# Optimization experiments

Measured on AMD Instinct MI355X. Metric: run time of the kernel, lower is better.

Reference implementation:

```python
import jax, jax.numpy as jnp
import numpy as np

D = 6          # atom_dims
K_AA = 17      # atom-atom knn (self dropped -> 16)
K_PE = 16      # point-atom knn
NEG = 0.2      # LeakyReLU slope
EPS = 1e-5     # GroupNorm eps
N_PTS, N_AT = 20000, 8000
H = 2 * D + 1  # MLP hidden width = 13


def lrelu(x):
    return jnp.where(x >= 0, x, NEG * x)


def linear(x, w, b):  # torch Linear convention: w is (out, in)
    return jnp.einsum('...i,oi->...o', x, w) + b


def group_norm(x, gamma, beta, groups):
    n, c = x.shape
    xg = x.reshape(n, groups, c // groups)
    mu = xg.mean(-1, keepdims=True)
    var = ((xg - mu) ** 2).mean(-1, keepdims=True)
    xn = ((xg - mu) * jax.lax.rsqrt(var + EPS)).reshape(n, c)
    return xn * gamma + beta


def knn(x, y, k):
    # squared euclidean distances via gram trick (memory-bound argKmin)
    d2 = jnp.sum(x * x, -1)[:, None] + jnp.sum(y * y, -1)[None, :] - 2.0 * (x @ y.T)
    _, idx = jax.lax.top_k(-jax.lax.stop_gradient(d2), k)
    # recompute dists from gathered coords (matches knn_atoms; differentiable)
    dists = jnp.sum((x[:, None, :] - y[idx]) ** 2, -1)  # (N, k)
    return idx, dists


def mp_block(self_feat, nb_source, idx, dists, w1, b1, w2, b2, gamma, beta, groups):
    n, k = idx.shape
    nb = nb_source[idx]  # (N, k, D) gather
    feat = jnp.concatenate([
        jnp.broadcast_to(self_feat[:, None, :], (n, k, self_feat.shape[1])),
        nb,
        dists[..., None],
    ], axis=-1)  # (N, k, 2D+1)
    msg = linear(lrelu(linear(feat, w1, b1)), w2, b2).sum(1)  # (N, D)
    return self_feat + lrelu(group_norm(msg, gamma, beta, groups))


def setup_inputs() -> dict:
    key = jax.random.key(0)
    ks = jax.random.split(key, 20)
    f = lambda k, s, sc=1.0: jax.random.normal(k, s, jnp.float32) * sc
    inp = {
        'xyz': f(ks[0], (N_PTS, 3), 10.0),
        'atom_xyz': f(ks[1], (N_AT, 3), 10.0),
        'atomtypes': f(ks[2], (N_AT, D)),
        'batch': jnp.zeros((N_PTS,), jnp.int32),
        'atom_batch': jnp.zeros((N_AT,), jnp.int32),
        # transform_types: Linear(D,D) -> LeakyReLU -> Linear(D,D)
        'tt_w1': f(ks[3], (D, D), 0.3), 'tt_b1': f(ks[4], (D,), 0.1),
        'tt_w2': f(ks[5], (D, D), 0.3), 'tt_b2': f(ks[6], (D,), 0.1),
        # atom_atom: 3 layers of Linear(13,13)->LeakyReLU->Linear(13,6), GroupNorm(2,6)
        'aa_w1': f(ks[7], (3, H, H), 0.3), 'aa_b1': f(ks[8], (3, H), 0.1),
        'aa_w2': f(ks[9], (3, D, H), 0.3), 'aa_b2': f(ks[10], (3, D), 0.1),
        'aa_gamma': jnp.ones((3, D), jnp.float32), 'aa_beta': jnp.zeros((3, D), jnp.float32),
        # embed: same shapes
        'em_w1': f(ks[11], (3, H, H), 0.3), 'em_b1': f(ks[12], (3, H), 0.1),
        'em_w2': f(ks[13], (3, D, H), 0.3), 'em_b2': f(ks[14], (3, D), 0.1),
        'em_gamma': jnp.ones((3, D), jnp.float32), 'em_beta': jnp.zeros((3, D), jnp.float32),
    }
    return inp


def reference(xyz, atom_xyz, atomtypes, batch, atom_batch,
              tt_w1, tt_b1, tt_w2, tt_b2,
              aa_w1, aa_b1, aa_w2, aa_b2, aa_gamma, aa_beta,
              em_w1, em_b1, em_w2, em_b2, em_gamma, em_beta):
    # batch / atom_batch are all-zero (single block), so full knn == ranged knn
    at = linear(lrelu(linear(atomtypes, tt_w1, tt_b1)), tt_w2, tt_b2)
    # Atom_Atom_embedding_MP: knn over atoms, drop self (first) neighbor
    idx, dists = knn(atom_xyz, atom_xyz, K_AA)
    idx, dists = idx[:, 1:], dists[:, 1:]
    out = at
    for i in range(3):
        out = mp_block(out, out, idx, dists,
                       aa_w1[i], aa_b1[i], aa_w2[i], aa_b2[i],
                       aa_gamma[i], aa_beta[i], 2)
    # Atom_embedding_MP: points gather from (fixed) atom features
    idx2, dists2 = knn(xyz, atom_xyz, K_PE)
    emb = jnp.ones((xyz.shape[0], D), xyz.dtype)
    for i in range(3):
        emb = mp_block(emb, out, idx2, dists2,
                       em_w1[i], em_b1[i], em_w2[i], em_b2[i],
                       em_gamma[i], em_beta[i], 2)
    return emb
```

## Files before the change

kernel.cpp:

```cpp
#include <hip/hip_runtime.h>
#include <cfloat>
#include <climits>

#define NEG 0.2f
#define GEPS 1e-5f
#define D 6
#define H 13
#define KOUT 16

#define MPAD 8192
#define TILE 1024
#define NTILES 8
#define QW 8
#define QBLK 32
#define CAP 64
#define KMAX 17
#define MARGIN 0.05f

__device__ __forceinline__ float lrelu(float x){ return x >= 0.f ? x : NEG*x; }

__global__ void pack_kernel(const float* __restrict__ xyz,
                            float4* __restrict__ P, int n, int npad){
  int i = blockIdx.x*blockDim.x + threadIdx.x;
  if (i >= npad) return;
  if (i < n){
    float x = xyz[3*i], y = xyz[3*i+1], z = xyz[3*i+2];
    float sq;
    {
#pragma clang fp contract(off)
      sq = (x*x + y*y) + z*z;
    }
    P[i] = make_float4(x,y,z,sq);
  } else {
    P[i] = make_float4(0.f,0.f,0.f,1e30f);
  }
}

__global__ void tt_kernel(const float* __restrict__ at_in,
                          const float* __restrict__ w1, const float* __restrict__ b1,
                          const float* __restrict__ w2, const float* __restrict__ b2,
                          float* __restrict__ out, int n){
  int i = blockIdx.x*blockDim.x + threadIdx.x;
  if (i >= n) return;
  float x[D], h[D];
  #pragma unroll
  for (int j=0;j<D;j++) x[j] = at_in[i*D+j];
  #pragma unroll
  for (int o=0;o<D;o++){
    float acc = b1[o];
    #pragma unroll
    for (int j=0;j<D;j++) acc += w1[o*D+j]*x[j];
    h[o] = lrelu(acc);
  }
  #pragma unroll
  for (int o=0;o<D;o++){
    float acc = b2[o];
    #pragma unroll
    for (int j=0;j<D;j++) acc += w2[o*D+j]*h[j];
    out[i*D+o] = acc;
  }
}

__device__ __forceinline__ void sort64fq(float (&v)[QW], int lane){
  #pragma unroll
  for (int k = 2; k <= 64; k <<= 1){
    #pragma unroll
    for (int j = k >> 1; j >= 1; j >>= 1){
      bool dir = ((lane & j) == 0) == ((lane & k) == 0);
      #pragma unroll
      for (int q = 0; q < QW; ++q){
        float o = __shfl_xor(v[q], j);
        v[q] = dir ? fminf(v[q], o) : fmaxf(v[q], o);
      }
    }
  }
}

__device__ __forceinline__ void sort64pair(float& d, int& i, int lane){
  #pragma unroll
  for (int k = 2; k <= 64; k <<= 1){
    #pragma unroll
    for (int j = k >> 1; j >= 1; j >>= 1){
      float od = __shfl_xor(d, j);
      int   oi = __shfl_xor(i, j);
      bool lower = (lane & j) == 0;
      bool asc   = (lane & k) == 0;
      bool oless = (od < d) || (od == d && oi < i);
      bool take  = (lower == asc) ? oless : !oless;
      d = take ? od : d;
      i = take ? oi : i;
    }
  }
}

__global__ __launch_bounds__(256)
void knn9_kernel(const float4* __restrict__ candP, int ncand,
                 const float4* __restrict__ qarrA, int nqA, int nbA,
                 const float4* __restrict__ qarrB, int nqB,
                 int* __restrict__ oidxA, float* __restrict__ odistA,
                 int* __restrict__ oidxB, float* __restrict__ odistB){
  __shared__ float4 tile[TILE];
  __shared__ float4 qs[QBLK];
  __shared__ ushort slots[4][QW][CAP];
  __shared__ int    scnt[4][QW];

  const int tid  = threadIdx.x;
  const int w    = tid >> 6;
  const int lane = tid & 63;

  const bool taskA = (int)blockIdx.x < nbA;
  const int  bq    = taskA ? blockIdx.x : (blockIdx.x - nbA);
  const float4* __restrict__ qarr = taskA ? qarrA : qarrB;
  const int  nq    = taskA ? nqA : nqB;
  const int  ksel  = taskA ? 17 : 16;
  const int  ooff  = taskA ? 1  : 0;
  int*   __restrict__ oidx  = taskA ? oidxA  : oidxB;
  float* __restrict__ odist = taskA ? odistA : odistB;

  if (tid < QBLK){
    int qg = bq*QBLK + tid;
    qs[tid] = qarr[qg < nq ? qg : nq-1];
  }
  if (lane < QW) scnt[w][lane] = 0;
  __syncthreads();

  float q2x[QW], q2y[QW], q2z[QW];
  #pragma unroll
  for (int q = 0; q < QW; ++q){
    float4 v = qs[w*QW + q];
    q2x[q] = -2.f*v.x; q2y[q] = -2.f*v.y; q2z[q] = -2.f*v.z;
  }

  float mn[QW];
  #pragma unroll
  for (int q = 0; q < QW; ++q) mn[q] = FLT_MAX;

  for (int t = 0; t < NTILES; ++t){
    #pragma unroll
    for (int u = 0; u < TILE/256; ++u)
      tile[tid + 256*u] = candP[t*TILE + tid + 256*u];
    __syncthreads();
    #pragma unroll 2
    for (int i = 0; i < TILE/64; ++i){
      float4 cv = tile[i*64 + lane];
      #pragma unroll
      for (int q = 0; q < QW; ++q){
        float e = fmaf(q2x[q], cv.x, fmaf(q2y[q], cv.y, fmaf(q2z[q], cv.z, cv.w)));
        mn[q] = fminf(mn[q], e);
      }
    }
    __syncthreads();
  }

  sort64fq(mn, lane);
  float T[QW];
  #pragma unroll
  for (int q = 0; q < QW; ++q) T[q] = __shfl(mn[q], ksel-1) + MARGIN;

  for (int t = 0; t < NTILES; ++t){
    #pragma unroll
    for (int u = 0; u < TILE/256; ++u)
      tile[tid + 256*u] = candP[t*TILE + tid + 256*u];
    __syncthreads();
    #pragma unroll 2
    for (int i = 0; i < TILE/64; ++i){
      float4 cv = tile[i*64 + lane];
      const int j = t*TILE + i*64 + lane;
      #pragma unroll
      for (int q = 0; q < QW; ++q){
        float e = fmaf(q2x[q], cv.x, fmaf(q2y[q], cv.y, fmaf(q2z[q], cv.z, cv.w)));
        if (e <= T[q]){
          int ofs = atomicAdd(&scnt[w][q], 1);
          if (ofs < CAP) slots[w][q][ofs] = (ushort)j;
        }
      }
    }
    __syncthreads();
  }

  for (int q = 0; q < QW; ++q){
    const int qgq = bq*QBLK + w*QW + q;
    if (qgq >= nq) continue;
    const float4 qv = qs[w*QW + q];
    const int C = scnt[w][q];

    if (C <= CAP){
      int g = INT_MAX; float d2 = FLT_MAX;
      if (lane < C){
        g = slots[w][q][lane];
        float4 cp = candP[g];
        {
#pragma clang fp contract(off)
          float dot = qv.x*cp.x + qv.y*cp.y + qv.z*cp.z;
          d2 = (qv.w + cp.w) - 2.0f*dot;
        }
      }
      sort64pair(d2, g, lane);
      if (lane >= ooff && lane < ooff + KOUT){
        float4 cp = candP[g];
        float dist;
        {
#pragma clang fp contract(off)
          float dx = qv.x-cp.x, dy = qv.y-cp.y, dz = qv.z-cp.z;
          dist = (dx*dx + dy*dy) + dz*dz;
        }
        oidx[(size_t)qgq*KOUT + (lane-ooff)]  = g;
        odist[(size_t)qgq*KOUT + (lane-ooff)] = dist;
      }
    } else if (lane == 0){
      float bd[KMAX]; int bi[KMAX];
      for (int t=0;t<ksel;t++){ bd[t]=FLT_MAX; bi[t]=INT_MAX; }
      float cmd = FLT_MAX; int cmi = INT_MAX;
      for (int jj = 0; jj < ncand; ++jj){
        float4 cp = candP[jj];
        float d2;
        {
#pragma clang fp contract(off)
          float dot = qv.x*cp.x + qv.y*cp.y + qv.z*cp.z;
          d2 = (qv.w + cp.w) - 2.0f*dot;
        }
        if (d2 < cmd || (d2 == cmd && jj < cmi)){
          int rt = 0; float rmd=-FLT_MAX; int rmi=-1;
          for (int t=0;t<ksel;t++){
            if (bd[t] > rmd || (bd[t]==rmd && bi[t]>rmi)){ rmd=bd[t]; rmi=bi[t]; rt=t; }
          }
          bd[rt]=d2; bi[rt]=jj;
          cmd=-FLT_MAX; cmi=-1;
          for (int t=0;t<ksel;t++){
            if (bd[t] > cmd || (bd[t]==cmd && bi[t]>cmi)){ cmd=bd[t]; cmi=bi[t]; }
          }
        }
      }
      for (int t=0;t<ksel;t++){
        int rt=-1; float mnd=FLT_MAX; int mni=INT_MAX;
        for (int u2=0;u2<ksel;u2++){
          if (bd[u2] < mnd || (bd[u2]==mnd && bi[u2]<mni)){ mnd=bd[u2]; mni=bi[u2]; rt=u2; }
        }
        bd[rt]=FLT_MAX; bi[rt]=INT_MAX;
        if (t >= ooff){
          float4 cp = candP[mni];
          float dist;
          {
#pragma clang fp contract(off)
            float dx=qv.x-cp.x, dy=qv.y-cp.y, dz=qv.z-cp.z;
            dist = (dx*dx + dy*dy) + dz*dz;
          }
          oidx[(size_t)qgq*KOUT + (t-ooff)]  = mni;
          odist[(size_t)qgq*KOUT + (t-ooff)] = dist;
        }
      }
    }
  }
}

template<bool SELF_ONES>
__global__ __launch_bounds__(256)
void mp_kernel(const float* __restrict__ self_feat,
               const float* __restrict__ nb_src,
               const int* __restrict__ idx,
               const float* __restrict__ dists,
               const float* __restrict__ w1g, const float* __restrict__ b1g,
               const float* __restrict__ w2g, const float* __restrict__ b2g,
               const float* __restrict__ gam, const float* __restrict__ bet,
               float* __restrict__ out, int n){
  __shared__ float w1[H*H], b1v[H], w2[D*H], b2v[D], gm[D], bt[D];
  for (int t=threadIdx.x; t<H*H; t+=blockDim.x) w1[t]=w1g[t];
  if (threadIdx.x < H) b1v[threadIdx.x]=b1g[threadIdx.x];
  for (int t=threadIdx.x; t<D*H; t+=blockDim.x) w2[t]=w2g[t];
  if (threadIdx.x < D){
    b2v[threadIdx.x]=b2g[threadIdx.x];
    gm[threadIdx.x]=gam[threadIdx.x];
    bt[threadIdx.x]=bet[threadIdx.x];
  }
  __syncthreads();
  int tt = blockIdx.x*blockDim.x + threadIdx.x;
  int p = tt >> 2, sub = tt & 3;
  if (p >= n) return;

  float s[D];
  #pragma unroll
  for (int j=0;j<D;j++) s[j] = SELF_ONES ? 1.0f : self_feat[p*D+j];
  float msg[D] = {0,0,0,0,0,0};

  #pragma unroll
  for (int u=0;u<KOUT/4;u++){
    int k = u*4 + sub;
    int j = idx[p*KOUT+k];
    float dd = dists[p*KOUT+k];
    float f[H];
    #pragma unroll
    for (int c=0;c<D;c++) f[c]=s[c];
    #pragma unroll
    for (int c=0;c<D;c++) f[D+c]=nb_src[j*D+c];
    f[2*D]=dd;
    float h[H];
    #pragma unroll
    for (int o=0;o<H;o++){
      float acc=b1v[o];
      #pragma unroll
      for (int c=0;c<H;c++) acc += w1[o*H+c]*f[c];
      h[o]=lrelu(acc);
    }
    #pragma unroll
    for (int o=0;o<D;o++){
      float acc=b2v[o];
      #pragma unroll
      for (int c=0;c<H;c++) acc += w2[o*H+c]*h[c];
      msg[o]+=acc;
    }
  }

  #pragma unroll
  for (int c=0;c<D;c++){
    msg[c] += __shfl_xor(msg[c], 1);
    msg[c] += __shfl_xor(msg[c], 2);
  }

  if (sub == 0){
    float y[D];
    #pragma unroll
    for (int gi=0; gi<2; gi++){
      float m0=msg[gi*3+0], m1=msg[gi*3+1], m2=msg[gi*3+2];
      float mu = ((m0+m1)+m2) / 3.0f;
      float d0=m0-mu, d1=m1-mu, d2v=m2-mu;
      float var = ((d0*d0 + d1*d1) + d2v*d2v) / 3.0f;
      float inv = 1.0f / sqrtf(var + GEPS);
      y[gi*3+0] = d0*inv;
      y[gi*3+1] = d1*inv;
      y[gi*3+2] = d2v*inv;
    }
    #pragma unroll
    for (int c=0;c<D;c++){
      float vv = y[c]*gm[c] + bt[c];
      out[p*D+c] = s[c] + lrelu(vv);
    }
  }
}

extern "C" void kernel_launch(void* const* d_in, const int* in_sizes, int n_in,
                              void* d_out, int out_size, void* d_ws, size_t ws_size,
                              hipStream_t stream){
  const float* xyz       = (const float*)d_in[0];
  const float* atom_xyz  = (const float*)d_in[1];
  const float* atomtypes = (const float*)d_in[2];
  const float* tt_w1 = (const float*)d_in[5];
  const float* tt_b1 = (const float*)d_in[6];
  const float* tt_w2 = (const float*)d_in[7];
  const float* tt_b2 = (const float*)d_in[8];
  const float* aa_w1 = (const float*)d_in[9];
  const float* aa_b1 = (const float*)d_in[10];
  const float* aa_w2 = (const float*)d_in[11];
  const float* aa_b2 = (const float*)d_in[12];
  const float* aa_gamma = (const float*)d_in[13];
  const float* aa_beta  = (const float*)d_in[14];
  const float* em_w1 = (const float*)d_in[15];
  const float* em_b1 = (const float*)d_in[16];
  const float* em_w2 = (const float*)d_in[17];
  const float* em_b2 = (const float*)d_in[18];
  const float* em_gamma = (const float*)d_in[19];
  const float* em_beta  = (const float*)d_in[20];

  const int n_pts = in_sizes[0]/3;
  const int n_at  = in_sizes[1]/3;

  char* ws = (char*)d_ws;
  float4* candP = (float4*)ws; ws += (size_t)MPAD*sizeof(float4);
  float4* ptsP  = (float4*)ws; ws += (size_t)n_pts*sizeof(float4);
  float* fa   = (float*)ws; ws += (size_t)n_at*D*4;
  float* fb   = (float*)ws; ws += (size_t)n_at*D*4;
  int*   idxA = (int*)ws;   ws += (size_t)n_at*KOUT*4;
  float* distA= (float*)ws; ws += (size_t)n_at*KOUT*4;
  int*   idxP = (int*)ws;   ws += (size_t)n_pts*KOUT*4;
  float* distP= (float*)ws; ws += (size_t)n_pts*KOUT*4;
  float* ea   = (float*)ws; ws += (size_t)n_pts*D*4;
  float* eb   = (float*)ws; ws += (size_t)n_pts*D*4;
  float* outf = (float*)d_out;

  pack_kernel<<<(MPAD+255)/256,256,0,stream>>>(atom_xyz, candP, n_at, MPAD);
  pack_kernel<<<(n_pts+255)/256,256,0,stream>>>(xyz, ptsP, n_pts, n_pts);

  tt_kernel<<<(n_at+255)/256,256,0,stream>>>(atomtypes, tt_w1,tt_b1,tt_w2,tt_b2, fa, n_at);

  const int nbA = (n_at  + QBLK - 1) / QBLK;
  const int nbB = (n_pts + QBLK - 1) / QBLK;
  knn9_kernel<<<nbA + nbB,256,0,stream>>>(
      candP, n_at, candP, n_at, nbA, ptsP, n_pts,
      idxA, distA, idxP, distP);

  mp_kernel<false><<<(n_at*4+255)/256,256,0,stream>>>(fa, fa, idxA, distA,
      aa_w1+0*H*H, aa_b1+0*H, aa_w2+0*D*H, aa_b2+0*D, aa_gamma+0*D, aa_beta+0*D, fb, n_at);
  mp_kernel<false><<<(n_at*4+255)/256,256,0,stream>>>(fb, fb, idxA, distA,
      aa_w1+1*H*H, aa_b1+1*H, aa_w2+1*D*H, aa_b2+1*D, aa_gamma+1*D, aa_beta+1*D, fa, n_at);
  mp_kernel<false><<<(n_at*4+255)/256,256,0,stream>>>(fa, fa, idxA, distA,
      aa_w1+2*H*H, aa_b1+2*H, aa_w2+2*D*H, aa_b2+2*D, aa_gamma+2*D, aa_beta+2*D, fb, n_at);

  mp_kernel<true ><<<(n_pts*4+255)/256,256,0,stream>>>(nullptr, fb, idxP, distP,
      em_w1+0*H*H, em_b1+0*H, em_w2+0*D*H, em_b2+0*D, em_gamma+0*D, em_beta+0*D, ea, n_pts);
  mp_kernel<false><<<(n_pts*4+255)/256,256,0,stream>>>(ea, fb, idxP, distP,
      em_w1+1*H*H, em_b1+1*H, em_w2+1*D*H, em_b2+1*D, em_gamma+1*D, em_beta+1*D, eb, n_pts);
  mp_kernel<false><<<(n_pts*4+255)/256,256,0,stream>>>(eb, fb, idxP, distP,
      em_w1+2*H*H, em_b1+2*H, em_w2+2*D*H, em_b2+2*D, em_gamma+2*D, em_beta+2*D, outf, n_pts);
}
```

Baseline: 162.9 us.

## Bound kNN threshold from half the candidates, add exact overflow fallback, fuse prep kernels

The first kNN pass now computes its per-query min-threshold from only the first 4 of 8 candidate tiles. That still gives a valid upper bound on the k-th distance but admits more candidates. When a query's candidate count overflows the slot capacity, a new per-query fallback rescans all candidates, computes an exact threshold, and compacts the survivors with ballot. The pack and type-transform kernels are merged into one prep kernel to save launches. The trade-off is cheaper pass 1 against a looser threshold, which makes overflow and the slow fallback path more likely.

```diff
diff --git a/kernel.cpp b/kernel.cpp
--- a/kernel.cpp
+++ b/kernel.cpp
@@ -11,6 +11,7 @@
 #define MPAD 8192
 #define TILE 1024
 #define NTILES 8
+#define P1TILES 4
 #define QW 8
 #define QBLK 32
 #define CAP 64
@@ -19,45 +20,54 @@
 
 __device__ __forceinline__ float lrelu(float x){ return x >= 0.f ? x : NEG*x; }
 
-__global__ void pack_kernel(const float* __restrict__ xyz,
-                            float4* __restrict__ P, int n, int npad){
+__global__ void prep_kernel(const float* __restrict__ atom_xyz,
+                            const float* __restrict__ xyz,
+                            const float* __restrict__ at_in,
+                            const float* __restrict__ w1, const float* __restrict__ b1,
+                            const float* __restrict__ w2, const float* __restrict__ b2,
+                            float4* __restrict__ candP, float4* __restrict__ ptsP,
+                            float* __restrict__ fa, int n_at, int n_pts){
   int i = blockIdx.x*blockDim.x + threadIdx.x;
-  if (i >= npad) return;
-  if (i < n){
+  if (i < MPAD){
+    if (i < n_at){
+      float x = atom_xyz[3*i], y = atom_xyz[3*i+1], z = atom_xyz[3*i+2];
+      float sq;
+      {
+#pragma clang fp contract(off)
+        sq = (x*x + y*y) + z*z;
+      }
+      candP[i] = make_float4(x,y,z,sq);
+    } else {
+      candP[i] = make_float4(0.f,0.f,0.f,1e30f);
+    }
+  }
+  if (i < n_pts){
     float x = xyz[3*i], y = xyz[3*i+1], z = xyz[3*i+2];
     float sq;
     {
 #pragma clang fp contract(off)
       sq = (x*x + y*y) + z*z;
     }
-    P[i] = make_float4(x,y,z,sq);
-  } else {
-    P[i] = make_float4(0.f,0.f,0.f,1e30f);
-  }
-}
-
-__global__ void tt_kernel(const float* __restrict__ at_in,
-                          const float* __restrict__ w1, const float* __restrict__ b1,
-                          const float* __restrict__ w2, const float* __restrict__ b2,
-                          float* __restrict__ out, int n){
-  int i = blockIdx.x*blockDim.x + threadIdx.x;
-  if (i >= n) return;
-  float x[D], h[D];
-  #pragma unroll
-  for (int j=0;j<D;j++) x[j] = at_in[i*D+j];
-  #pragma unroll
-  for (int o=0;o<D;o++){
-    float acc = b1[o];
-    #pragma unroll
-    for (int j=0;j<D;j++) acc += w1[o*D+j]*x[j];
-    h[o] = lrelu(acc);
-  }
-  #pragma unroll
-  for (int o=0;o<D;o++){
-    float acc = b2[o];
-    #pragma unroll
-    for (int j=0;j<D;j++) acc += w2[o*D+j]*h[j];
-    out[i*D+o] = acc;
+    ptsP[i] = make_float4(x,y,z,sq);
+  }
+  if (i < n_at){
+    float x[D], h[D];
+    #pragma unroll
+    for (int j=0;j<D;j++) x[j] = at_in[i*D+j];
+    #pragma unroll
+    for (int o=0;o<D;o++){
+      float acc = b1[o];
+      #pragma unroll
+      for (int j=0;j<D;j++) acc += w1[o*D+j]*x[j];
+      h[o] = lrelu(acc);
+    }
+    #pragma unroll
+    for (int o=0;o<D;o++){
+      float acc = b2[o];
+      #pragma unroll
+      for (int j=0;j<D;j++) acc += w2[o*D+j]*h[j];
+      fa[i*D+o] = acc;
+    }
   }
 }
 
@@ -72,6 +82,18 @@
         float o = __shfl_xor(v[q], j);
         v[q] = dir ? fminf(v[q], o) : fmaxf(v[q], o);
       }
+    }
+  }
+}
+
+__device__ __forceinline__ void sort64f1(float& a, int lane){
+  #pragma unroll
+  for (int k=2;k<=64;k<<=1){
+    #pragma unroll
+    for (int j=k>>1;j>=1;j>>=1){
+      float o = __shfl_xor(a, j);
+      bool dir = ((lane&j)==0)==((lane&k)==0);
+      a = dir ? fminf(a,o) : fmaxf(a,o);
     }
   }
 }
@@ -94,11 +116,11 @@
 }
 
 __global__ __launch_bounds__(256)
-void knn9_kernel(const float4* __restrict__ candP, int ncand,
-                 const float4* __restrict__ qarrA, int nqA, int nbA,
-                 const float4* __restrict__ qarrB, int nqB,
-                 int* __restrict__ oidxA, float* __restrict__ odistA,
-                 int* __restrict__ oidxB, float* __restrict__ odistB){
+void knn10_kernel(const float4* __restrict__ candP, int ncand,
+                  const float4* __restrict__ qarrA, int nqA, int nbA,
+                  const float4* __restrict__ qarrB, int nqB,
+                  int* __restrict__ oidxA, float* __restrict__ odistA,
+                  int* __restrict__ oidxB, float* __restrict__ odistB){
   __shared__ float4 tile[TILE];
   __shared__ float4 qs[QBLK];
   __shared__ ushort slots[4][QW][CAP];
@@ -135,7 +157,7 @@
   #pragma unroll
   for (int q = 0; q < QW; ++q) mn[q] = FLT_MAX;
 
-  for (int t = 0; t < NTILES; ++t){
+  for (int t = 0; t < P1TILES; ++t){
     #pragma unroll
     for (int u = 0; u < TILE/256; ++u)
       tile[tid + 256*u] = candP[t*TILE + tid + 256*u];
@@ -182,7 +204,34 @@
     const int qgq = bq*QBLK + w*QW + q;
     if (qgq >= nq) continue;
     const float4 qv = qs[w*QW + q];
-    const int C = scnt[w][q];
+    int C = scnt[w][q];
+
+    if (C > CAP){
+      const float fq2x = -2.f*qv.x, fq2y = -2.f*qv.y, fq2z = -2.f*qv.z;
+      float m = FLT_MAX;
+      for (int j = lane; j < MPAD; j += 64){
+        float4 cp = candP[j];
+        float e = fmaf(fq2x, cp.x, fmaf(fq2y, cp.y, fmaf(fq2z, cp.z, cp.w)));
+        m = fminf(m, e);
+      }
+      sort64f1(m, lane);
+      const float T2 = __shfl(m, ksel-1) + MARGIN;
+      int cnt = 0;
+      const unsigned long long ltm = (1ULL << lane) - 1ULL;
+      for (int j = lane; j < MPAD; j += 64){
+        float4 cp = candP[j];
+        float e = fmaf(fq2x, cp.x, fmaf(fq2y, cp.y, fmaf(fq2z, cp.z, cp.w)));
+        bool acc = e <= T2;
+        unsigned long long msk = __ballot(acc);
+        if (acc){
+          int ofs = cnt + __popcll(msk & ltm);
+          if (ofs < CAP) slots[w][q][ofs] = (ushort)j;
+        }
+        cnt += __popcll(msk);
+      }
+      __threadfence_block();
+      C = cnt;
+    }
 
     if (C <= CAP){
       int g = INT_MAX; float d2 = FLT_MAX;
@@ -376,14 +425,14 @@
   float* eb   = (float*)ws; ws += (size_t)n_pts*D*4;
   float* outf = (float*)d_out;
 
-  pack_kernel<<<(MPAD+255)/256,256,0,stream>>>(atom_xyz, candP, n_at, MPAD);
-  pack_kernel<<<(n_pts+255)/256,256,0,stream>>>(xyz, ptsP, n_pts, n_pts);
-
-  tt_kernel<<<(n_at+255)/256,256,0,stream>>>(atomtypes, tt_w1,tt_b1,tt_w2,tt_b2, fa, n_at);
+  const int nprep = (MPAD > n_pts ? MPAD : n_pts);
+  prep_kernel<<<(nprep+255)/256,256,0,stream>>>(
+      atom_xyz, xyz, atomtypes, tt_w1, tt_b1, tt_w2, tt_b2,
+      candP, ptsP, fa, n_at, n_pts);
 
   const int nbA = (n_at  + QBLK - 1) / QBLK;
   const int nbB = (n_pts + QBLK - 1) / QBLK;
-  knn9_kernel<<<nbA + nbB,256,0,stream>>>(
+  knn10_kernel<<<nbA + nbB,256,0,stream>>>(
       candP, n_at, candP, n_at, nbA, ptsP, n_pts,
       idxA, distA, idxP, distP);
 
```

Result: slower. 179.3 us (+10.1%).
